# Performance work log

Hardware: AMD Instinct MI355X
Metric: run time of the kernel (lower is better)

Reference implementation:

```python
import jax, jax.numpy as jnp
import numpy as np
import math

HIDDEN = 1024
HEADS = 16

def setup_inputs() -> dict:
    key = jax.random.key(0)
    k1, k2, k3 = jax.random.split(key, 3)
    B, T, C = 4, 2048, HIDDEN
    x = jax.random.normal(k1, (B, T, C), dtype=jnp.float32)
    w_qkv = jax.random.normal(k2, (C, 3 * C), dtype=jnp.float32) * (1.0 / math.sqrt(C))
    b_qkv = jnp.zeros((3 * C,), dtype=jnp.float32)
    w_out = jax.random.normal(k3, (C, C), dtype=jnp.float32) * (1.0 / math.sqrt(C))
    b_out = jnp.zeros((C,), dtype=jnp.float32)
    return {"x": x, "w_qkv": w_qkv, "b_qkv": b_qkv, "w_out": w_out, "b_out": b_out}

def reference(x, w_qkv, b_qkv, w_out, b_out):
    B, T, C = x.shape
    H = HEADS
    D = C // H  # head dim
    qkv = x @ w_qkv + b_qkv  # [B,T,3C]
    q, k, v = jnp.split(qkv, 3, axis=2)
    # [B,T,C] -> [B,H,T,D]
    q = q.reshape(B, T, H, D).transpose(0, 2, 1, 3)
    k = k.reshape(B, T, H, D).transpose(0, 2, 1, 3)
    v = v.reshape(B, T, H, D).transpose(0, 2, 1, 3)
    scale = 1.0 / math.sqrt(D)
    logits = jnp.einsum('bhqd,bhkd->bhqk', q, k) * scale  # [B,H,T,T]
    causal = jnp.tril(jnp.ones((T, T), dtype=bool))
    logits = jnp.where(causal[None, None, :, :], logits, -jnp.inf)
    probs = jax.nn.softmax(logits, axis=-1)
    out = jnp.einsum('bhqk,bhkd->bhqd', probs, v)  # [B,H,T,D]
    out = out.transpose(0, 2, 1, 3).reshape(B, T, C)
    return out @ w_out + b_out
```

## Files before the change

### kernel.cpp

```cpp
#include <hip/hip_runtime.h>
#include <hip/hip_bf16.h>

#define C_DIM  1024
#define NHEAD  16
#define DHEAD  64
#define T_LEN  2048
#define B_SZ   4
#define M_ROWS (B_SZ * T_LEN)
#define QKV_N  (3 * C_DIM)

typedef __bf16 bf16x8 __attribute__((ext_vector_type(8)));
typedef float  f32x4  __attribute__((ext_vector_type(4)));
typedef unsigned short ushort8_t __attribute__((ext_vector_type(8)));
typedef unsigned int   uint4_t   __attribute__((ext_vector_type(4)));
typedef short          short4_t  __attribute__((ext_vector_type(4)));

#if __has_builtin(__builtin_amdgcn_mfma_f32_16x16x16bf16_1k)
#define HAVE_MFMA_X16 1
#else
#define HAVE_MFMA_X16 0
#endif

__device__ __forceinline__ unsigned short f2bf(float f) {
    union { float f; unsigned int u; } v; v.f = f;
    unsigned int r = v.u + 0x7FFFu + ((v.u >> 16) & 1u);
    return (unsigned short)(r >> 16);
}

__device__ __forceinline__ bf16x8 as_bf16x8(ushort8_t u) {
    return __builtin_bit_cast(bf16x8, u);
}

__device__ __forceinline__ f32x4 mfma16(bf16x8 a, bf16x8 b, f32x4 c) {
    return __builtin_amdgcn_mfma_f32_16x16x32_bf16(a, b, c, 0, 0, 0);
}

#define GLL16(gsrc, ldst) __builtin_amdgcn_global_load_lds( \
    (const __attribute__((address_space(1))) void*)(gsrc),  \
    (__attribute__((address_space(3))) void*)(ldst), 16, 0, 0)

__device__ __forceinline__ int xcd_remap(int id, int nwg) {
    const int q = nwg >> 3, r = nwg & 7;
    const int xcd = id & 7, off = id >> 3;
    return (xcd < r) ? (xcd * (q + 1) + off) : (r * (q + 1) + (xcd - r) * q + off);
}

__global__ void k_prep(const float* __restrict__ x,
                       const float* __restrict__ wqkv, const float* __restrict__ wout,
                       unsigned short* __restrict__ xb,
                       unsigned short* __restrict__ wqkvT, unsigned short* __restrict__ woutT) {
    __shared__ float tile[32][33];
    const int bid = blockIdx.x;
    const int tid = threadIdx.x;

    if (bid < 8192) {
        const int i = bid * 256 + tid;
        const float4 v = ((const float4*)x)[i];
        unsigned int lo = (unsigned int)f2bf(v.x) | ((unsigned int)f2bf(v.y) << 16);
        unsigned int hi = (unsigned int)f2bf(v.z) | ((unsigned int)f2bf(v.w) << 16);
        ((uint2*)xb)[i] = make_uint2(lo, hi);
        return;
    }

    const int tb  = bid - 8192;
    const int bxr = tb & 127;
    const int ky  = tb >> 7;
    const bool isQ = (bxr < QKV_N / 32);
    const int bx = isQ ? bxr : bxr - QKV_N / 32;
    const float* w = isQ ? wqkv : wout;
    unsigned short* wT = isQ ? wqkvT : woutT;
    const int N = isQ ? QKV_N : C_DIM;
    const int K = C_DIM;

    const int n0 = bx * 32, k0 = ky * 32;
    const int tx = tid & 31, ty = tid >> 5;
    for (int i = 0; i < 32; i += 8)
        tile[ty + i][tx] = w[(size_t)(k0 + ty + i) * N + (n0 + tx)];
    __syncthreads();
    for (int i = 0; i < 32; i += 8)
        wT[(size_t)(n0 + ty + i) * K + (k0 + tx)] = f2bf(tile[tx][ty + i]);
}

__global__ void k_transpose_v(const unsigned short* __restrict__ qkv,
                              unsigned short* __restrict__ vtg) {
    __shared__ unsigned short tile[32][33];
    const int tt = blockIdx.x;
    const int dy = blockIdx.y;
    const int bh = dy >> 1, dtile = dy & 1;
    const int b = bh >> 4, h = bh & 15;
    const int t0 = tt * 32, d0 = dtile * 32;
    const int tx = threadIdx.x, ty = threadIdx.y;
    const unsigned short* src = qkv + (size_t)b * T_LEN * QKV_N + 2 * C_DIM + h * DHEAD + d0;
    for (int i = 0; i < 32; i += 8)
        tile[ty + i][tx] = src[(size_t)(t0 + ty + i) * QKV_N + tx];
    __syncthreads();
    unsigned short* dst = vtg + ((size_t)bh * DHEAD + d0) * T_LEN + t0;
    for (int i = 0; i < 32; i += 8)
        dst[(size_t)(ty + i) * T_LEN + tx] = tile[tx][ty + i];
}

template<int BF16_OUT>
__global__ __launch_bounds__(256) void k_gemm(const unsigned short* __restrict__ A,
                       const unsigned short* __restrict__ Bt,
                       const float* __restrict__ bias,
                       void* __restrict__ C,
                       unsigned short* __restrict__ vtg,
                       int M, int N, int K) {
    __shared__ unsigned short As[128][64];
    __shared__ unsigned short Bs[128][64];

    const int tid  = threadIdx.x;
    const int lane = tid & 63;
    const int wv   = tid >> 6;
    const int wm = wv >> 1, wn = wv & 1;

    const int nwg = gridDim.x * gridDim.y;
    const int wg  = xcd_remap(blockIdx.y * gridDim.x + blockIdx.x, nwg);
    const int bx = wg % gridDim.x, by = wg / gridDim.x;
    const int m0 = by * 128;
    const int n0 = bx * 128;
    const int lr = lane & 15, lg = lane >> 4;

    f32x4 acc[4][4];
#pragma unroll
    for (int i = 0; i < 4; i++)
#pragma unroll
        for (int j = 0; j < 4; j++) acc[i][j] = (f32x4){0.f, 0.f, 0.f, 0.f};

    const int gr = lane >> 3;
    const int gc = 8 * ((lane & 7) ^ gr);

    for (int kt = 0; kt < K; kt += 64) {
        __syncthreads();
#pragma unroll
        for (int j = 0; j < 4; j++) {
            const int row = 32 * wv + 8 * j;
            GLL16(A  + (size_t)(m0 + row + gr) * K + kt + gc, &As[row][0]);
            GLL16(Bt + (size_t)(n0 + row + gr) * K + kt + gc, &Bs[row][0]);
        }
        __syncthreads();

#pragma unroll
        for (int s = 0; s < 2; s++) {
            const int cb = (s * 64 + lg * 16) ^ ((lr & 7) << 4);
            bf16x8 af[4], bfr[4];
#pragma unroll
            for (int i = 0; i < 4; i++)
                af[i] = as_bf16x8(*(const ushort8_t*)((const char*)&As[wm * 64 + i * 16 + lr][0] + cb));
#pragma unroll
            for (int j = 0; j < 4; j++)
                bfr[j] = as_bf16x8(*(const ushort8_t*)((const char*)&Bs[wn * 64 + j * 16 + lr][0] + cb));
#pragma unroll
            for (int i = 0; i < 4; i++)
#pragma unroll
                for (int j = 0; j < 4; j++)
                    acc[i][j] = mfma16(af[i], bfr[j], acc[i][j]);
        }
    }

    const bool isV = (vtg != nullptr) && (n0 >= 2 * C_DIM);
#pragma unroll
    for (int i = 0; i < 4; i++) {
#pragma unroll
        for (int j = 0; j < 4; j++) {
            const int col = n0 + wn * 64 + j * 16 + lr;
            const float bv = bias ? bias[col] : 0.f;
            if (isV) {
                const int dcol = col - 2 * C_DIM;
                const int hh = dcol >> 6, dd = dcol & 63;
                const int row0 = m0 + wm * 64 + i * 16 + lg * 4;
                const int bb = row0 >> 11, t0 = row0 & (T_LEN - 1);
                const unsigned int p0 = (unsigned int)f2bf(acc[i][j][0] + bv)
                                      | ((unsigned int)f2bf(acc[i][j][1] + bv) << 16);
                const unsigned int p1 = (unsigned int)f2bf(acc[i][j][2] + bv)
                                      | ((unsigned int)f2bf(acc[i][j][3] + bv) << 16);
                *(uint2*)&vtg[(((size_t)(bb * 16 + hh)) * 64 + dd) * T_LEN + t0] = make_uint2(p0, p1);
            } else {
#pragma unroll
                for (int r = 0; r < 4; r++) {
                    const int row = m0 + wm * 64 + i * 16 + lg * 4 + r;
                    const float v = acc[i][j][r] + bv;
                    if (BF16_OUT)
                        ((unsigned short*)C)[(size_t)row * N + col] = f2bf(v);
                    else
                        ((float*)C)[(size_t)row * N + col] = v;
                }
            }
        }
    }
}

#define KS_OFF(B_, ROW_) (((B_) << 13) + ((ROW_) << 7))
#define VS_OFF(B_, ROW_) (16384 + ((B_) << 13) + ((ROW_) << 7))
#define SCALE2 0.180336880f
__global__ __launch_bounds__(256, 4) void k_attn(const unsigned short* __restrict__ qkv,
                                                 const unsigned short* __restrict__ vtg,
                                                 unsigned short* __restrict__ out) {
    __shared__ __align__(16) char asmem[32768];

    const int blk = xcd_remap(blockIdx.x, B_SZ * NHEAD * 16);
    const int pr = blk & 15;
    const int h  = (blk >> 4) & 15;
    const int b  = blk >> 8;
    const int bh = b * 16 + h;

    const int tid  = threadIdx.x;
    const int lane = tid & 63;
    const int w    = tid >> 6;
    const int lr = lane & 15, lg = lane >> 4;
    const int gr = lane >> 3;
    const int gc = 8 * ((lane & 7) ^ gr);
    const int ra = w * 16;

    const size_t base = (size_t)b * T_LEN * QKV_N + (size_t)h * DHEAD;
    const unsigned short* Qp = qkv + base;
    const unsigned short* Kp = qkv + base + C_DIM;
    const unsigned short* Vt = vtg + (size_t)bh * DHEAD * T_LEN;

    int buf = 0;
    for (int t = 0; t < 2; t++) {
        const int qt = (t == 0) ? pr : (31 - pr);
        const int qw = qt * 64 + w * 16;
        const int qg = qw + lr;
        const int R  = qt + 1;

        bf16x8 qf[2];
#pragma unroll
        for (int s = 0; s < 2; s++)
            qf[s] = as_bf16x8(*(const ushort8_t*)&Qp[(size_t)(qw + lr) * QKV_N + s * 32 + lg * 8]);

        f32x4 o[4];
#pragma unroll
        for (int f = 0; f < 4; f++) o[f] = (f32x4){0.f, 0.f, 0.f, 0.f};
        float lp = 0.f;

        GLL16(Kp + (size_t)(ra + gr) * QKV_N + gc,          asmem + KS_OFF(buf, ra));
        GLL16(Kp + (size_t)(ra + 8 + gr) * QKV_N + gc,      asmem + KS_OFF(buf, ra + 8));
        GLL16(Vt + (size_t)(ra + gr) * T_LEN + gc,          asmem + VS_OFF(buf, ra));
        GLL16(Vt + (size_t)(ra + 8 + gr) * T_LEN + gc,      asmem + VS_OFF(buf, ra + 8));

        for (int r = 0; r < R; ++r) {
            const int kb = r * 64;

            asm volatile("s_waitcnt vmcnt(0)" ::: "memory");
            __builtin_amdgcn_s_barrier();
            __builtin_amdgcn_sched_barrier(0);

            if (r + 1 < R) {
                const int kn = kb + 64;
                GLL16(Kp + (size_t)(kn + ra + gr) * QKV_N + gc,     asmem + KS_OFF(buf ^ 1, ra));
                GLL16(Kp + (size_t)(kn + ra + 8 + gr) * QKV_N + gc, asmem + KS_OFF(buf ^ 1, ra + 8));
                GLL16(Vt + (size_t)(ra + gr) * T_LEN + kn + gc,     asmem + VS_OFF(buf ^ 1, ra));
                GLL16(Vt + (size_t)(ra + 8 + gr) * T_LEN + kn + gc, asmem + VS_OFF(buf ^ 1, ra + 8));
            }

            f32x4 s4[4];
            __builtin_amdgcn_s_setprio(1);
#pragma unroll
            for (int f = 0; f < 4; f++) {
                const int row = f * 16 + lr;
                const bf16x8 kf0 = as_bf16x8(*(const ushort8_t*)
                    (asmem + KS_OFF(buf, row) + ((lg * 16) ^ ((lr & 7) << 4))));
                const bf16x8 kf1 = as_bf16x8(*(const ushort8_t*)
                    (asmem + KS_OFF(buf, row) + ((64 + lg * 16) ^ ((lr & 7) << 4))));
                f32x4 s = (f32x4){0.f, 0.f, 0.f, 0.f};
                s = mfma16(kf0, qf[0], s);
                s = mfma16(kf1, qf[1], s);
                s4[f] = s;
            }
            __builtin_amdgcn_s_setprio(0);

            const bool last = (r == R - 1);
            unsigned int pb[4][2];
#pragma unroll
            for (int f = 0; f < 4; f++) {
                unsigned short hh[4];
#pragma unroll
                for (int rr = 0; rr < 4; rr++) {
                    float sv = fminf(s4[f][rr] * SCALE2, 72.f);
                    if (last) {
                        const int kg = kb + f * 16 + lg * 4 + rr;
                        if (kg > qg) sv = -1e30f;
                    }
                    const float e = __builtin_amdgcn_exp2f(sv);
                    lp += e;
                    hh[rr] = __builtin_bit_cast(unsigned short, (__bf16)e);
                }
                pb[f][0] = (unsigned int)hh[0] | ((unsigned int)hh[1] << 16);
                pb[f][1] = (unsigned int)hh[2] | ((unsigned int)hh[3] << 16);
            }

            __builtin_amdgcn_s_setprio(1);
#pragma unroll
            for (int kg = 0; kg < 4; kg++) {
#if HAVE_MFMA_X16
                const short4_t pbv = __builtin_bit_cast(short4_t,
                    make_uint2(pb[kg][0], pb[kg][1]));
#else
                uint4_t pw;
                pw.x = pb[kg][0]; pw.y = pb[kg][1]; pw.z = 0u; pw.w = 0u;
                const bf16x8 pbv8 = __builtin_bit_cast(bf16x8, pw);
#endif
#pragma unroll
                for (int fd = 0; fd < 4; fd++) {
                    const int drow = fd * 16 + lr;
                    const uint2 va = *(const uint2*)(asmem + VS_OFF(buf, drow) +
                                     ((kg * 32 + lg * 8) ^ ((lr & 7) << 4)));
#if HAVE_MFMA_X16
                    o[fd] = __builtin_amdgcn_mfma_f32_16x16x16bf16_1k(
                        __builtin_bit_cast(short4_t, va), pbv, o[fd], 0, 0, 0);
#else
                    uint4_t vw;
                    vw.x = va.x; vw.y = va.y; vw.z = va.x; vw.w = va.y;
                    o[fd] = mfma16(__builtin_bit_cast(bf16x8, vw), pbv8, o[fd]);
#endif
                }
            }
            __builtin_amdgcn_s_setprio(0);

            buf ^= 1;
        }

        lp += __shfl_xor(lp, 16, 64);
        lp += __shfl_xor(lp, 32, 64);
        const float inv = 1.f / lp;

        unsigned short* orow = out + ((size_t)b * T_LEN + qw + lr) * C_DIM + h * DHEAD;
#pragma unroll
        for (int fd = 0; fd < 4; fd++) {
            const unsigned int p0 = (unsigned int)f2bf(o[fd][0] * inv)
                                  | ((unsigned int)f2bf(o[fd][1] * inv) << 16);
            const unsigned int p1 = (unsigned int)f2bf(o[fd][2] * inv)
                                  | ((unsigned int)f2bf(o[fd][3] * inv) << 16);
            *(uint2*)&orow[fd * 16 + lg * 4] = make_uint2(p0, p1);
        }
    }
}

extern "C" void kernel_launch(void* const* d_in, const int* in_sizes, int n_in,
                              void* d_out, int out_size, void* d_ws, size_t ws_size,
                              hipStream_t stream) {
    const float* x      = (const float*)d_in[0];
    const float* w_qkv  = (const float*)d_in[1];
    const float* b_qkv  = (const float*)d_in[2];
    const float* w_out  = (const float*)d_in[3];
    const float* b_out  = (const float*)d_in[4];
    float* out = (float*)d_out;

    char* ws = (char*)d_ws;
    unsigned short* xb    = (unsigned short*)(ws);
    unsigned short* wqkvT = (unsigned short*)(ws + 16777216);
    unsigned short* woutT = (unsigned short*)(ws + 16777216 + 6291456);
    unsigned short* qkv   = (unsigned short*)(ws + 25165824);
    unsigned short* attn  = (unsigned short*)(ws + 75497472);

    const size_t VTG_OFF = 92274688ull;
    const bool fused_vt = (ws_size >= VTG_OFF + 16777216ull);
    unsigned short* vtg = fused_vt ? (unsigned short*)(ws + VTG_OFF)
                                   : (unsigned short*)(ws);

    k_prep<<<8192 + 4096, 256, 0, stream>>>(x, w_qkv, w_out, xb, wqkvT, woutT);
    k_gemm<1><<<dim3(QKV_N / 128, M_ROWS / 128), 256, 0, stream>>>(
        xb, wqkvT, b_qkv, qkv, fused_vt ? vtg : nullptr, M_ROWS, QKV_N, C_DIM);
    if (!fused_vt)
        k_transpose_v<<<dim3(T_LEN / 32, 64 * 2), dim3(32, 8), 0, stream>>>(qkv, vtg);
    k_attn<<<B_SZ * NHEAD * 16, 256, 0, stream>>>(qkv, vtg, attn);
    k_gemm<0><<<dim3(C_DIM / 128, M_ROWS / 128), 256, 0, stream>>>(
        attn, woutT, b_out, out, nullptr, M_ROWS, C_DIM, C_DIM);
}
```

Before: 166.1 us.

## Process both causal query tiles in one pass sharing K/V tile loads

Merges the two sequential query-tile passes (tile pr and tile 31-pr) into one loop over the longer key range, computing both tiles against each loaded K/V tile while the shorter tile is still active. This removes duplicate global-to-LDS loads and barriers for the overlapping key range and gives more independent MFMA work per iteration. It doubles accumulator and Q-fragment registers, which may reduce occupancy or cause spills.

```diff
diff --git a/kernel.cpp b/kernel.cpp
--- a/kernel.cpp
+++ b/kernel.cpp
@@ -217,123 +217,168 @@
     const unsigned short* Kp = qkv + base + C_DIM;
     const unsigned short* Vt = vtg + (size_t)bh * DHEAD * T_LEN;
 
+    const int qta = pr, qtb = 31 - pr;
+    const int Ra = qta + 1;
+    const int Rm = qtb + 1;
+    const int qwa = qta * 64 + w * 16, qga = qwa + lr;
+    const int qwb = qtb * 64 + w * 16, qgb = qwb + lr;
+
+    bf16x8 qfa[2], qfb[2];
+#pragma unroll
+    for (int s = 0; s < 2; s++) {
+        qfa[s] = as_bf16x8(*(const ushort8_t*)&Qp[(size_t)(qwa + lr) * QKV_N + s * 32 + lg * 8]);
+        qfb[s] = as_bf16x8(*(const ushort8_t*)&Qp[(size_t)(qwb + lr) * QKV_N + s * 32 + lg * 8]);
+    }
+
+    f32x4 oa[4], ob[4];
+#pragma unroll
+    for (int f = 0; f < 4; f++) {
+        oa[f] = (f32x4){0.f, 0.f, 0.f, 0.f};
+        ob[f] = (f32x4){0.f, 0.f, 0.f, 0.f};
+    }
+    float lpa = 0.f, lpb = 0.f;
+
     int buf = 0;
-    for (int t = 0; t < 2; t++) {
-        const int qt = (t == 0) ? pr : (31 - pr);
-        const int qw = qt * 64 + w * 16;
-        const int qg = qw + lr;
-        const int R  = qt + 1;
-
-        bf16x8 qf[2];
-#pragma unroll
-        for (int s = 0; s < 2; s++)
-            qf[s] = as_bf16x8(*(const ushort8_t*)&Qp[(size_t)(qw + lr) * QKV_N + s * 32 + lg * 8]);
-
-        f32x4 o[4];
-#pragma unroll
-        for (int f = 0; f < 4; f++) o[f] = (f32x4){0.f, 0.f, 0.f, 0.f};
-        float lp = 0.f;
-
-        GLL16(Kp + (size_t)(ra + gr) * QKV_N + gc,          asmem + KS_OFF(buf, ra));
-        GLL16(Kp + (size_t)(ra + 8 + gr) * QKV_N + gc,      asmem + KS_OFF(buf, ra + 8));
-        GLL16(Vt + (size_t)(ra + gr) * T_LEN + gc,          asmem + VS_OFF(buf, ra));
-        GLL16(Vt + (size_t)(ra + 8 + gr) * T_LEN + gc,      asmem + VS_OFF(buf, ra + 8));
-
-        for (int r = 0; r < R; ++r) {
-            const int kb = r * 64;
-
-            asm volatile("s_waitcnt vmcnt(0)" ::: "memory");
-            __builtin_amdgcn_s_barrier();
-            __builtin_amdgcn_sched_barrier(0);
-
-            if (r + 1 < R) {
-                const int kn = kb + 64;
-                GLL16(Kp + (size_t)(kn + ra + gr) * QKV_N + gc,     asmem + KS_OFF(buf ^ 1, ra));
-                GLL16(Kp + (size_t)(kn + ra + 8 + gr) * QKV_N + gc, asmem + KS_OFF(buf ^ 1, ra + 8));
-                GLL16(Vt + (size_t)(ra + gr) * T_LEN + kn + gc,     asmem + VS_OFF(buf ^ 1, ra));
-                GLL16(Vt + (size_t)(ra + 8 + gr) * T_LEN + kn + gc, asmem + VS_OFF(buf ^ 1, ra + 8));
+    GLL16(Kp + (size_t)(ra + gr) * QKV_N + gc,          asmem + KS_OFF(buf, ra));
+    GLL16(Kp + (size_t)(ra + 8 + gr) * QKV_N + gc,      asmem + KS_OFF(buf, ra + 8));
+    GLL16(Vt + (size_t)(ra + gr) * T_LEN + gc,          asmem + VS_OFF(buf, ra));
+    GLL16(Vt + (size_t)(ra + 8 + gr) * T_LEN + gc,      asmem + VS_OFF(buf, ra + 8));
+
+    for (int r = 0; r < Rm; ++r) {
+        const int kb = r * 64;
+
+        asm volatile("s_waitcnt vmcnt(0)" ::: "memory");
+        __builtin_amdgcn_s_barrier();
+        __builtin_amdgcn_sched_barrier(0);
+
+        if (r + 1 < Rm) {
+            const int kn = kb + 64;
+            GLL16(Kp + (size_t)(kn + ra + gr) * QKV_N + gc,     asmem + KS_OFF(buf ^ 1, ra));
+            GLL16(Kp + (size_t)(kn + ra + 8 + gr) * QKV_N + gc, asmem + KS_OFF(buf ^ 1, ra + 8));
+            GLL16(Vt + (size_t)(ra + gr) * T_LEN + kn + gc,     asmem + VS_OFF(buf ^ 1, ra));
+            GLL16(Vt + (size_t)(ra + 8 + gr) * T_LEN + kn + gc, asmem + VS_OFF(buf ^ 1, ra + 8));
+        }
+
+        const bool aact = (r < Ra);
+
+        f32x4 s4a[4], s4b[4];
+        __builtin_amdgcn_s_setprio(1);
+#pragma unroll
+        for (int f = 0; f < 4; f++) {
+            const int row = f * 16 + lr;
+            const bf16x8 kf0 = as_bf16x8(*(const ushort8_t*)
+                (asmem + KS_OFF(buf, row) + ((lg * 16) ^ ((lr & 7) << 4))));
+            const bf16x8 kf1 = as_bf16x8(*(const ushort8_t*)
+                (asmem + KS_OFF(buf, row) + ((64 + lg * 16) ^ ((lr & 7) << 4))));
+            f32x4 s = (f32x4){0.f, 0.f, 0.f, 0.f};
+            s = mfma16(kf0, qfb[0], s);
+            s = mfma16(kf1, qfb[1], s);
+            s4b[f] = s;
+            if (aact) {
+                f32x4 t = (f32x4){0.f, 0.f, 0.f, 0.f};
+                t = mfma16(kf0, qfa[0], t);
+                t = mfma16(kf1, qfa[1], t);
+                s4a[f] = t;
             }
-
-            f32x4 s4[4];
-            __builtin_amdgcn_s_setprio(1);
-#pragma unroll
-            for (int f = 0; f < 4; f++) {
-                const int row = f * 16 + lr;
-                const bf16x8 kf0 = as_bf16x8(*(const ushort8_t*)
-                    (asmem + KS_OFF(buf, row) + ((lg * 16) ^ ((lr & 7) << 4))));
-                const bf16x8 kf1 = as_bf16x8(*(const ushort8_t*)
-                    (asmem + KS_OFF(buf, row) + ((64 + lg * 16) ^ ((lr & 7) << 4))));
-                f32x4 s = (f32x4){0.f, 0.f, 0.f, 0.f};
-                s = mfma16(kf0, qf[0], s);
-                s = mfma16(kf1, qf[1], s);
-                s4[f] = s;
+        }
+        __builtin_amdgcn_s_setprio(0);
+
+        const bool lastb = (r == Rm - 1);
+        const bool lasta = (r == Ra - 1);
+        unsigned int pbb[4][2], pba[4][2];
+#pragma unroll
+        for (int f = 0; f < 4; f++) {
+            unsigned short hh[4];
+#pragma unroll
+            for (int rr = 0; rr < 4; rr++) {
+                float sv = fminf(s4b[f][rr] * SCALE2, 72.f);
+                if (lastb) {
+                    const int kg = kb + f * 16 + lg * 4 + rr;
+                    if (kg > qgb) sv = -1e30f;
+                }
+                const float e = __builtin_amdgcn_exp2f(sv);
+                lpb += e;
+                hh[rr] = __builtin_bit_cast(unsigned short, (__bf16)e);
             }
-            __builtin_amdgcn_s_setprio(0);
-
-            const bool last = (r == R - 1);
-            unsigned int pb[4][2];
+            pbb[f][0] = (unsigned int)hh[0] | ((unsigned int)hh[1] << 16);
+            pbb[f][1] = (unsigned int)hh[2] | ((unsigned int)hh[3] << 16);
+        }
+        if (aact) {
 #pragma unroll
             for (int f = 0; f < 4; f++) {
                 unsigned short hh[4];
 #pragma unroll
                 for (int rr = 0; rr < 4; rr++) {
-                    float sv = fminf(s4[f][rr] * SCALE2, 72.f);
-                    if (last) {
+                    float sv = fminf(s4a[f][rr] * SCALE2, 72.f);
+                    if (lasta) {
                         const int kg = kb + f * 16 + lg * 4 + rr;
-                        if (kg > qg) sv = -1e30f;
+                        if (kg > qga) sv = -1e30f;
                     }
                     const float e = __builtin_amdgcn_exp2f(sv);
-                    lp += e;
+                    lpa += e;
                     hh[rr] = __builtin_bit_cast(unsigned short, (__bf16)e);
                 }
-                pb[f][0] = (unsigned int)hh[0] | ((unsigned int)hh[1] << 16);
-                pb[f][1] = (unsigned int)hh[2] | ((unsigned int)hh[3] << 16);
+                pba[f][0] = (unsigned int)hh[0] | ((unsigned int)hh[1] << 16);
+                pba[f][1] = (unsigned int)hh[2] | ((unsigned int)hh[3] << 16);
             }
-
-            __builtin_amdgcn_s_setprio(1);
-#pragma unroll
-            for (int kg = 0; kg < 4; kg++) {
+        }
+
+        __builtin_amdgcn_s_setprio(1);
+#pragma unroll
+        for (int kg = 0; kg < 4; kg++) {
 #if HAVE_MFMA_X16
-                const short4_t pbv = __builtin_bit_cast(short4_t,
-                    make_uint2(pb[kg][0], pb[kg][1]));
+            const short4_t pvb = __builtin_bit_cast(short4_t, make_uint2(pbb[kg][0], pbb[kg][1]));
+            const short4_t pva = __builtin_bit_cast(short4_t, make_uint2(pba[kg][0], pba[kg][1]));
 #else
-                uint4_t pw;
-                pw.x = pb[kg][0]; pw.y = pb[kg][1]; pw.z = 0u; pw.w = 0u;
-                const bf16x8 pbv8 = __builtin_bit_cast(bf16x8, pw);
+            uint4_t pwb; pwb.x = pbb[kg][0]; pwb.y = pbb[kg][1]; pwb.z = 0u; pwb.w = 0u;
+            const bf16x8 pvb8 = __builtin_bit_cast(bf16x8, pwb);
+            uint4_t pwa; pwa.x = pba[kg][0]; pwa.y = pba[kg][1]; pwa.z = 0u; pwa.w = 0u;
+            const bf16x8 pva8 = __builtin_bit_cast(bf16x8, pwa);
 #endif
 #pragma unroll
-                for (int fd = 0; fd < 4; fd++) {
-                    const int drow = fd * 16 + lr;
-                    const uint2 va = *(const uint2*)(asmem + VS_OFF(buf, drow) +
-                                     ((kg * 32 + lg * 8) ^ ((lr & 7) << 4)));
+            for (int fd = 0; fd < 4; fd++) {
+                const int drow = fd * 16 + lr;
+                const uint2 va = *(const uint2*)(asmem + VS_OFF(buf, drow) +
+                                 ((kg * 32 + lg * 8) ^ ((lr & 7) << 4)));
 #if HAVE_MFMA_X16
-                    o[fd] = __builtin_amdgcn_mfma_f32_16x16x16bf16_1k(
-                        __builtin_bit_cast(short4_t, va), pbv, o[fd], 0, 0, 0);
+                const short4_t vas = __builtin_bit_cast(short4_t, va);
+                ob[fd] = __builtin_amdgcn_mfma_f32_16x16x16bf16_1k(vas, pvb, ob[fd], 0, 0, 0);
+                if (aact)
+                    oa[fd] = __builtin_amdgcn_mfma_f32_16x16x16bf16_1k(vas, pva, oa[fd], 0, 0, 0);
 #else
-                    uint4_t vw;
-                    vw.x = va.x; vw.y = va.y; vw.z = va.x; vw.w = va.y;
-                    o[fd] = mfma16(__builtin_bit_cast(bf16x8, vw), pbv8, o[fd]);
+                uint4_t vw; vw.x = va.x; vw.y = va.y; vw.z = va.x; vw.w = va.y;
+                const bf16x8 vd = __builtin_bit_cast(bf16x8, vw);
+                ob[fd] = mfma16(vd, pvb8, ob[fd]);
+                if (aact) oa[fd] = mfma16(vd, pva8, oa[fd]);
 #endif
-                }
             }
-            __builtin_amdgcn_s_setprio(0);
-
-            buf ^= 1;
-        }
-
-        lp += __shfl_xor(lp, 16, 64);
-        lp += __shfl_xor(lp, 32, 64);
-        const float inv = 1.f / lp;
-
-        unsigned short* orow = out + ((size_t)b * T_LEN + qw + lr) * C_DIM + h * DHEAD;
-#pragma unroll
-        for (int fd = 0; fd < 4; fd++) {
-            const unsigned int p0 = (unsigned int)f2bf(o[fd][0] * inv)
-                                  | ((unsigned int)f2bf(o[fd][1] * inv) << 16);
-            const unsigned int p1 = (unsigned int)f2bf(o[fd][2] * inv)
-                                  | ((unsigned int)f2bf(o[fd][3] * inv) << 16);
-            *(uint2*)&orow[fd * 16 + lg * 4] = make_uint2(p0, p1);
-        }
+        }
+        __builtin_amdgcn_s_setprio(0);
+
+        buf ^= 1;
+    }
+
+    lpa += __shfl_xor(lpa, 16, 64);
+    lpa += __shfl_xor(lpa, 32, 64);
+    lpb += __shfl_xor(lpb, 16, 64);
+    lpb += __shfl_xor(lpb, 32, 64);
+    const float inva = 1.f / lpa;
+    const float invb = 1.f / lpb;
+
+    unsigned short* orowa = out + ((size_t)b * T_LEN + qwa + lr) * C_DIM + h * DHEAD;
+    unsigned short* orowb = out + ((size_t)b * T_LEN + qwb + lr) * C_DIM + h * DHEAD;
+#pragma unroll
+    for (int fd = 0; fd < 4; fd++) {
+        unsigned int p0 = (unsigned int)f2bf(oa[fd][0] * inva)
+                        | ((unsigned int)f2bf(oa[fd][1] * inva) << 16);
+        unsigned int p1 = (unsigned int)f2bf(oa[fd][2] * inva)
+                        | ((unsigned int)f2bf(oa[fd][3] * inva) << 16);
+        *(uint2*)&orowa[fd * 16 + lg * 4] = make_uint2(p0, p1);
+        p0 = (unsigned int)f2bf(ob[fd][0] * invb)
+           | ((unsigned int)f2bf(ob[fd][1] * invb) << 16);
+        p1 = (unsigned int)f2bf(ob[fd][2] * invb)
+           | ((unsigned int)f2bf(ob[fd][3] * invb) << 16);
+        *(uint2*)&orowb[fd * 16 + lg * 4] = make_uint2(p0, p1);
     }
 }
 
```

New measurement: 186.0 us. 1.12x slower.
